# Performance work log

Hardware: AMD Instinct MI355X
Metric: run time of the kernel (lower is better)

The kernel has to match this reference:

```python
import jax, jax.numpy as jnp
import numpy as np

B, F, M, N, H, O = 8, 128, 256, 1024, 64, 128
BN_EPS = 1e-5
COS_EPS = 1e-8


def _bn(x, g, b, m, v):
    # inference-mode BatchNorm over channel axis 1
    shape = [1] * x.ndim
    shape[1] = -1
    return g.reshape(shape) * (x - m.reshape(shape)) * jax.lax.rsqrt(v.reshape(shape) + BN_EPS) + b.reshape(shape)


def setup_inputs() -> dict:
    key = jax.random.key(0)
    ks = jax.random.split(key, 24)
    def n(k, shape, s=1.0):
        return jax.random.normal(k, shape, dtype=jnp.float32) * s
    inp = {}
    inp['template_feature'] = n(ks[0], (B, F, M))
    inp['search_feature'] = n(ks[1], (B, F, N))
    # SharedMLP 1x1 conv weights (bias=False because bn=True)
    inp['W1'] = n(ks[2], (H, F + 1), 0.05)
    inp['W2'] = n(ks[3], (H, H), 0.05)
    inp['W3'] = n(ks[4], (H, H), 0.05)
    # fea_layer: conv1d(H, bn=True) then conv1d(O, activation=None, bias=True)
    inp['Wc1'] = n(ks[5], (H, H), 0.05)
    inp['Wc2'] = n(ks[6], (O, H), 0.05)
    inp['bc2'] = n(ks[7], (O,), 0.05)
    for i, nm in enumerate(['1', '2', '3', 'c1']):
        inp['g' + nm] = 1.0 + n(ks[8 + i], (H,), 0.1)
        inp['b' + nm] = n(ks[12 + i], (H,), 0.1)
        inp['m' + nm] = n(ks[16 + i], (H,), 0.01)
        inp['v' + nm] = jax.random.uniform(ks[20 + i], (H,), minval=0.5, maxval=1.5, dtype=jnp.float32)
    return inp


def reference(template_feature, search_feature, W1, W2, W3, Wc1, Wc2, bc2,
              g1, b1, m1, v1, g2, b2, m2, v2, g3, b3, m3, v3, gc1, bc1, mc1, vc1):
    t, s = template_feature, search_feature
    # pairwise cosine similarity over channel dim (no BxFxMxN expand needed)
    dot = jnp.einsum('bfm,bfn->bmn', t, s)
    nt = jnp.linalg.norm(t, axis=1)  # (B, M)
    ns = jnp.linalg.norm(s, axis=1)  # (B, N)
    cos = dot / jnp.maximum(nt[:, :, None] * ns[:, None, :], COS_EPS)  # (B, M, N)
    # first 1x1 conv on concat(cos, expand(t)) computed fused (no concat materialization)
    h = jnp.einsum('hf,bfm->bhm', W1[:, 1:], t)[..., None] + W1[:, 0][None, :, None, None] * cos[:, None]
    h = jax.nn.relu(_bn(h, g1, b1, m1, v1))  # (B, H, M, N)
    h = jax.nn.relu(_bn(jnp.einsum('gh,bhmn->bgmn', W2, h), g2, b2, m2, v2))
    h = jax.nn.relu(_bn(jnp.einsum('gh,bhmn->bgmn', W3, h), g3, b3, m3, v3))
    p = jnp.max(h, axis=2)  # max-pool over M -> (B, H, N)
    c = jax.nn.relu(_bn(jnp.einsum('gh,bhn->bgn', Wc1, p), gc1, bc1, mc1, vc1))
    return jnp.einsum('oh,bhn->bon', Wc2, c) + bc2[None, :, None]  # (B, O, N)
```

## Files before the change

kernel.cpp:

```cpp
#include <hip/hip_runtime.h>


#define BB 8
#define FF 128
#define MM 256
#define NN 1024
#define HH 64
#define OO 128
#define BN_EPS 1e-5f
#define COS_EPS 1e-8f

#define WS_U     0
#define WS_C2    64
#define WS_C3    128
#define WS_CC1   192
#define WS_W2H   256
#define WS_W3H   2304
#define WS_WC1F  8448
#define WS_A1    12544
#define WS_NT    143616
#define WS_NS    145664
#define WS_COSH  153856
#define WS_P     1202432
#define PS       524288

typedef _Float16 half2v __attribute__((ext_vector_type(2)));
typedef _Float16 half8  __attribute__((ext_vector_type(8)));
typedef __attribute__((ext_vector_type(4))) float f32x4;

__device__ __forceinline__ unsigned int pkh2(float a, float b){
  auto h = __builtin_amdgcn_cvt_pkrtz(a, b);
  return __builtin_bit_cast(unsigned int, h);
}
__device__ __forceinline__ half2v u2h(unsigned int u){
  return __builtin_bit_cast(half2v, u);
}
__device__ __forceinline__ unsigned int h2u(half2v v){
  return __builtin_bit_cast(unsigned int, v);
}
__device__ __forceinline__ unsigned int relu2(unsigned int d){
  half2v v = __builtin_elementwise_max(u2h(d), (half2v){(_Float16)0, (_Float16)0});
  return h2u(v);
}
__device__ __forceinline__ unsigned int bh1(unsigned int up, half2v c, unsigned int ap){
  half2v v = __builtin_elementwise_fma(u2h(up), c, u2h(ap));
  v = __builtin_elementwise_max(v, (half2v){(_Float16)0, (_Float16)0});
  return h2u(v);
}
__device__ __forceinline__ float dot4(float4 a, float4 b, float acc){
  acc = fmaf(a.x, b.x, acc); acc = fmaf(a.y, b.y, acc);
  acc = fmaf(a.z, b.z, acc); acc = fmaf(a.w, b.w, acc);
  return acc;
}

__global__ __launch_bounds__(256) void k_prep(const float* t_, const float* s_,
    const float* W1, const float* W2, const float* W3, const float* Wc1,
    const float* g1, const float* b1, const float* m1, const float* v1,
    const float* g2, const float* b2, const float* m2, const float* v2,
    const float* g3, const float* b3, const float* m3, const float* v3,
    const float* gc1,const float* bc1,const float* mc1,const float* vc1,
    float* ws){
  __shared__ float W1s[64][133];
  int t = threadIdx.x;
  int bx = blockIdx.x;
  if (bx < 256){
    int b = bx >> 5, m0 = (bx & 31)*8;
    for (int idx = t; idx < 8192; idx += 256){
      int h = idx >> 7, f = idx & 127;
      W1s[h][f] = W1[h*129 + 1 + f];
    }
    __syncthreads();
    int h = t & 63, mg = t >> 6;
    const float* tp = t_ + (size_t)b*FF*MM + m0 + mg*2;
    float acc0 = 0.f, acc1 = 0.f;
    for (int f = 0; f < FF; f++){
      float wv = W1s[h][f];
      float2 tv = *(const float2*)&tp[(size_t)f*MM];
      acc0 = fmaf(wv, tv.x, acc0); acc1 = fmaf(wv, tv.y, acc1);
    }
    float a1 = g1[h] / sqrtf(v1[h] + BN_EPS);
    float c1 = b1[h] - a1*m1[h];
    unsigned short* dst = (unsigned short*)(ws + WS_A1) + ((size_t)(b*MM + m0 + mg*2))*64 + h;
    dst[0]  = (unsigned short)(pkh2(fmaf(a1, acc0, c1), 0.f) & 0xFFFFu);
    dst[64] = (unsigned short)(pkh2(fmaf(a1, acc1, c1), 0.f) & 0xFFFFu);
  } else if (bx < 416){
    __shared__ float red[4][64];
    int x = t & 63, fq = t >> 6;
    int idx = (bx - 256)*64 + x;
    const float* ptr; size_t stride;
    if (idx < BB*MM){
      int b = idx >> 8, m = idx & 255;
      ptr = t_ + (size_t)b*FF*MM + m; stride = MM;
    } else {
      int j = idx - BB*MM;
      int b = j >> 10, n = j & 1023;
      ptr = s_ + (size_t)b*FF*NN + n; stride = NN;
    }
    float acc = 0.f;
    for (int f = fq*32; f < fq*32 + 32; f++){
      float v = ptr[(size_t)f*stride]; acc = fmaf(v, v, acc);
    }
    red[fq][x] = acc;
    __syncthreads();
    if (fq == 0)
      ws[WS_NT + idx] = sqrtf(red[0][x] + red[1][x] + red[2][x] + red[3][x]);
  } else {
    if (t < 64){
      float a1 = g1[t] / sqrtf(v1[t] + BN_EPS);
      ws[WS_U + t]   = a1 * W1[t*129];
      float a2 = g2[t] / sqrtf(v2[t] + BN_EPS);
      ws[WS_C2 + t]  = b2[t] - a2*m2[t];
      float a3 = g3[t] / sqrtf(v3[t] + BN_EPS);
      ws[WS_C3 + t]  = b3[t] - a3*m3[t];
      float ac = gc1[t] / sqrtf(vc1[t] + BN_EPS);
      ws[WS_CC1 + t] = bc1[t] - ac*mc1[t];
    }
    unsigned short* w2h = (unsigned short*)(ws + WS_W2H);
    unsigned short* w3h = (unsigned short*)(ws + WS_W3H);
    for (int i = t; i < 4096; i += 256){
      int g = i >> 6;
      float a2 = g2[g] / sqrtf(v2[g] + BN_EPS);
      w2h[i] = __builtin_bit_cast(unsigned short, (_Float16)(a2 * W2[i]));
      float a3 = g3[g] / sqrtf(v3[g] + BN_EPS);
      w3h[i] = __builtin_bit_cast(unsigned short, (_Float16)(a3 * W3[i]));
      float ac = gc1[g] / sqrtf(vc1[g] + BN_EPS);
      ws[WS_WC1F + i] = ac * Wc1[i];
    }
  }
}

__global__ __launch_bounds__(256) void k_cos(const float* t_, const float* s_, float* ws){
  __shared__ __align__(16) unsigned short tS[64][136];
  __shared__ __align__(16) unsigned short sS[64][136];
  __shared__ float ntS[64], nsS[64];
  int t = threadIdx.x;
  int lane = t & 63, w = t >> 6;
  int ln15 = lane & 15, quad = lane >> 4;
  int m0 = blockIdx.x*64, n0 = blockIdx.y*64, b = blockIdx.z;
  {
    int x = t & 63;
    const float* tb = t_ + (size_t)b*FF*MM + m0 + x;
    const float* sb = s_ + (size_t)b*FF*NN + n0 + x;
    #pragma unroll
    for (int k = 0; k < 16; k++){
      int fp = w*16 + k;
      *(unsigned int*)&tS[x][2*fp] = pkh2(tb[(size_t)(2*fp)*MM], tb[(size_t)(2*fp+1)*MM]);
      *(unsigned int*)&sS[x][2*fp] = pkh2(sb[(size_t)(2*fp)*NN], sb[(size_t)(2*fp+1)*NN]);
    }
    if (t < 64) ntS[t] = ws[WS_NT + b*MM + m0 + t];
    else if (t < 128) nsS[t-64] = ws[WS_NS + b*NN + n0 + (t-64)];
  }
  __syncthreads();
  half8 A4[4];
  #pragma unroll
  for (int kc = 0; kc < 4; kc++)
    A4[kc] = *(const half8*)&tS[w*16 + ln15][kc*32 + quad*8];
  float4 nt4 = *(const float4*)&ntS[w*16 + quad*4];
  unsigned short* cosw = (unsigned short*)(ws + WS_COSH);
  #pragma unroll
  for (int ns = 0; ns < 4; ns++){
    f32x4 acc = (f32x4){0.f,0.f,0.f,0.f};
    #pragma unroll
    for (int kc = 0; kc < 4; kc++){
      half8 B4 = *(const half8*)&sS[ns*16 + ln15][kc*32 + quad*8];
      acc = __builtin_amdgcn_mfma_f32_16x16x32_f16(A4[kc], B4, acc, 0, 0, 0);
    }
    float nsv = nsS[ns*16 + ln15];
    int n = n0 + ns*16 + ln15;
    #pragma unroll
    for (int r = 0; r < 4; r++){
      int m = m0 + w*16 + quad*4 + r;
      float denom = fmaxf(nt4[r]*nsv, COS_EPS);
      float c = acc[r] * __builtin_amdgcn_rcpf(denom);
      cosw[(size_t)(b*MM + m)*NN + n] = (unsigned short)(pkh2(c, 0.f) & 0xFFFFu);
    }
  }
}

__global__ __launch_bounds__(256, 3) void k_main(const float* ws, float* Pp){
  __shared__ __align__(16) unsigned short h2W[4][16][72];
  __shared__ __align__(16) float redS[3][16][68];
  int t = threadIdx.x;
  int lane = t & 63, w = t >> 6;
  int ln15 = lane & 15, quad = lane >> 4;
  int b = blockIdx.y;
  int n0 = blockIdx.x * 16;
  int ms = blockIdx.z;

  const unsigned short* w2h = (const unsigned short*)(ws + WS_W2H);
  const unsigned short* w3h = (const unsigned short*)(ws + WS_W3H);
  half8 W2A[4][2], W3A[4][2];
  f32x4 c2v[4], c3v[4];
  #pragma unroll
  for (int rt = 0; rt < 4; rt++){
    int g = rt*16 + ln15;
    #pragma unroll
    for (int kk = 0; kk < 2; kk++){
      W2A[rt][kk] = *(const half8*)&w2h[g*64 + kk*32 + quad*8];
      W3A[rt][kk] = *(const half8*)&w3h[g*64 + kk*32 + quad*8];
    }
    float4 cb2 = *(const float4*)&ws[WS_C2 + rt*16 + quad*4];
    float4 cb3 = *(const float4*)&ws[WS_C3 + rt*16 + quad*4];
    c2v[rt] = (f32x4){cb2.x, cb2.y, cb2.z, cb2.w};
    c3v[rt] = (f32x4){cb3.x, cb3.y, cb3.z, cb3.w};
  }
  unsigned int upk[2][4];
  #pragma unroll
  for (int kk = 0; kk < 2; kk++){
    float4 ua = *(const float4*)&ws[WS_U + kk*32 + quad*8];
    float4 ub = *(const float4*)&ws[WS_U + kk*32 + quad*8 + 4];
    upk[kk][0] = pkh2(ua.x, ua.y); upk[kk][1] = pkh2(ua.z, ua.w);
    upk[kk][2] = pkh2(ub.x, ub.y); upk[kk][3] = pkh2(ub.z, ub.w);
  }
  const unsigned short* A1H = (const unsigned short*)(ws + WS_A1) + (size_t)b*MM*64;
  int n = n0 + ln15;
  const unsigned short* cosP = (const unsigned short*)(ws + WS_COSH)
                               + (size_t)b*MM*NN + n;
  unsigned short* h2w = &h2W[w][0][0];

  f32x4 p[4];
  #pragma unroll
  for (int rt = 0; rt < 4; rt++) p[rt] = (f32x4){0.f,0.f,0.f,0.f};

  int m0i = ms*128 + w;
  unsigned int cu = cosP[(size_t)m0i*NN];
  uint4 a1a = *(const uint4*)&A1H[(size_t)m0i*64 + quad*8];
  uint4 a1b = *(const uint4*)&A1H[(size_t)m0i*64 + 32 + quad*8];

  for (int mc = 0; mc < 32; mc++){
    int mN = ms*128 + (mc < 31 ? (mc + 1) : 31)*4 + w;
    unsigned int cuN = cosP[(size_t)mN*NN];
    uint4 a1aN = *(const uint4*)&A1H[(size_t)mN*64 + quad*8];
    uint4 a1bN = *(const uint4*)&A1H[(size_t)mN*64 + 32 + quad*8];

    unsigned int cd = cu | (cu << 16);
    half2v ch = u2h(cd);
    uint4 q0, q1;
    q0.x = bh1(upk[0][0], ch, a1a.x); q0.y = bh1(upk[0][1], ch, a1a.y);
    q0.z = bh1(upk[0][2], ch, a1a.z); q0.w = bh1(upk[0][3], ch, a1a.w);
    q1.x = bh1(upk[1][0], ch, a1b.x); q1.y = bh1(upk[1][1], ch, a1b.y);
    q1.z = bh1(upk[1][2], ch, a1b.z); q1.w = bh1(upk[1][3], ch, a1b.w);
    half8 b0h = __builtin_bit_cast(half8, q0);
    half8 b1h = __builtin_bit_cast(half8, q1);

    f32x4 acc[4];
    #pragma unroll
    for (int rt = 0; rt < 4; rt++){
      acc[rt] = __builtin_amdgcn_mfma_f32_16x16x32_f16(W2A[rt][0], b0h, c2v[rt], 0, 0, 0);
      acc[rt] = __builtin_amdgcn_mfma_f32_16x16x32_f16(W2A[rt][1], b1h, acc[rt], 0, 0, 0);
    }
    #pragma unroll
    for (int rt = 0; rt < 4; rt++){
      uint2 vv;
      vv.x = relu2(pkh2(acc[rt][0], acc[rt][1]));
      vv.y = relu2(pkh2(acc[rt][2], acc[rt][3]));
      *(uint2*)&h2w[ln15*72 + rt*16 + quad*4] = vv;
    }
    __asm__ volatile("s_waitcnt lgkmcnt(0)" ::: "memory");
    half8 e0 = *(const half8*)&h2w[ln15*72 + quad*8];
    half8 e1 = *(const half8*)&h2w[ln15*72 + 32 + quad*8];
    #pragma unroll
    for (int rt = 0; rt < 4; rt++){
      f32x4 a3 = __builtin_amdgcn_mfma_f32_16x16x32_f16(W3A[rt][0], e0, c3v[rt], 0, 0, 0);
      a3 = __builtin_amdgcn_mfma_f32_16x16x32_f16(W3A[rt][1], e1, a3, 0, 0, 0);
      #pragma unroll
      for (int r = 0; r < 4; r++) p[rt][r] = fmaxf(p[rt][r], a3[r]);
    }
    cu = cuN; a1a = a1aN; a1b = a1bN;
  }

  __syncthreads();
  if (w >= 1){
    #pragma unroll
    for (int rt = 0; rt < 4; rt++){
      f32x4 v = p[rt];
      *(float4*)&redS[w-1][ln15][rt*16 + quad*4] = make_float4(v[0], v[1], v[2], v[3]);
    }
  }
  __syncthreads();
  if (w == 0){
    float* Pb = Pp + (size_t)ms*PS + ((size_t)(b*NN + n) << 6);
    #pragma unroll
    for (int rt = 0; rt < 4; rt++){
      float4 o1 = *(const float4*)&redS[0][ln15][rt*16 + quad*4];
      float4 o2 = *(const float4*)&redS[1][ln15][rt*16 + quad*4];
      float4 o3 = *(const float4*)&redS[2][ln15][rt*16 + quad*4];
      float4 r4;
      r4.x = fmaxf(fmaxf(p[rt][0], o1.x), fmaxf(o2.x, o3.x));
      r4.y = fmaxf(fmaxf(p[rt][1], o1.y), fmaxf(o2.y, o3.y));
      r4.z = fmaxf(fmaxf(p[rt][2], o1.z), fmaxf(o2.z, o3.z));
      r4.w = fmaxf(fmaxf(p[rt][3], o1.w), fmaxf(o2.w, o3.w));
      *(float4*)&Pb[rt*16 + quad*4] = r4;
    }
  }
}

__global__ __launch_bounds__(256) void k_tail(const float* Wc2, const float* bc2,
                                              const float* ws, float* out){
  __shared__ float WT[64][68];
  __shared__ float pT[32][68];
  __shared__ float cS[32][68];
  int t = threadIdx.x;
  int n0 = blockIdx.x * 32;
  int b = blockIdx.y;
  for (int i = t; i < 4096; i += 256) WT[i >> 6][i & 63] = ws[WS_WC1F + i];
  const float* P0 = ws + WS_P + ((size_t)(b*NN + n0) << 6);
  const float* P1 = P0 + PS;
  for (int i = t; i < 2048; i += 256) pT[i >> 6][i & 63] = fmaxf(P0[i], P1[i]);
  __syncthreads();
  {
    int n = t & 31, q = t >> 5;
    for (int k = 0; k < 8; k++){
      int g = q*8 + k;
      float acc = ws[WS_CC1 + g];
      for (int hs = 0; hs < 64; hs += 4){
        float4 wv = *(const float4*)&WT[g][hs];
        float4 pv = *(const float4*)&pT[n][hs];
        acc = dot4(wv, pv, acc);
      }
      cS[n][g] = fmaxf(acc, 0.f);
    }
  }
  __syncthreads();
  {
    int o = t & 127, hf = t >> 7;
    float bco = bc2[o];
    float accO[16];
    #pragma unroll
    for (int i = 0; i < 16; i++) accO[i] = bco;
    for (int hs = 0; hs < 64; hs += 4){
      float4 w4 = *(const float4*)&Wc2[o*64 + hs];
      #pragma unroll
      for (int i = 0; i < 16; i++){
        float4 cv = *(const float4*)&cS[hf*16 + i][hs];
        accO[i] = dot4(w4, cv, accO[i]);
      }
    }
    #pragma unroll
    for (int i = 0; i < 16; i++)
      out[((size_t)(b*OO + o))*NN + n0 + hf*16 + i] = accO[i];
  }
}

extern "C" void kernel_launch(void* const* d_in, const int* in_sizes, int n_in,
                              void* d_out, int out_size, void* d_ws, size_t ws_size,
                              hipStream_t stream){
  (void)in_sizes; (void)n_in; (void)out_size; (void)ws_size;
  const float* t_  = (const float*)d_in[0];
  const float* s_  = (const float*)d_in[1];
  const float* W1  = (const float*)d_in[2];
  const float* W2  = (const float*)d_in[3];
  const float* W3  = (const float*)d_in[4];
  const float* Wc1 = (const float*)d_in[5];
  const float* Wc2 = (const float*)d_in[6];
  const float* bc2 = (const float*)d_in[7];
  const float* g1 = (const float*)d_in[8],  *b1 = (const float*)d_in[9],
             * m1 = (const float*)d_in[10], *v1 = (const float*)d_in[11];
  const float* g2 = (const float*)d_in[12], *b2 = (const float*)d_in[13],
             * m2 = (const float*)d_in[14], *v2 = (const float*)d_in[15];
  const float* g3 = (const float*)d_in[16], *b3 = (const float*)d_in[17],
             * m3 = (const float*)d_in[18], *v3 = (const float*)d_in[19];
  const float* gc1 = (const float*)d_in[20], *bc1 = (const float*)d_in[21],
             * mc1 = (const float*)d_in[22], *vc1 = (const float*)d_in[23];
  float* ws = (float*)d_ws;
  float* out = (float*)d_out;

  k_prep<<<417, 256, 0, stream>>>(t_, s_, W1, W2, W3, Wc1,
      g1,b1,m1,v1, g2,b2,m2,v2, g3,b3,m3,v3, gc1,bc1,mc1,vc1, ws);
  k_cos<<<dim3(4, 16, 8), 256, 0, stream>>>(t_, s_, ws);
  k_main<<<dim3(64, 8, 2), 256, 0, stream>>>(ws, ws + WS_P);
  k_tail<<<dim3(32, 8), 256, 0, stream>>>(Wc2, bc2, ws, out);
}
```

Baseline: 183.2 us.

## Software-pipeline layer2/layer3 MFMAs with double-buffered LDS and defer bias/ReLU past max

Restructures the per-warp M loop so that the layer-3 MFMAs for iteration mc-1 run while the layer-2 MFMAs for iteration mc are issued. Layer-2 results go into a double-buffered LDS staging area with a new padded byte layout, which removes the explicit lgkmcnt wait between the store and reload. The layer-3 bias and ReLU are moved out of the inner loop and applied once after the max reduction, since max commutes with a per-channel add and with ReLU. The running max is now initialised to a large negative value so this stays correct. The change adds a prologue and epilogue and more live registers, which may pressure occupancy under launch_bounds(256,3).

```diff
diff --git a/kernel.cpp b/kernel.cpp
--- a/kernel.cpp
+++ b/kernel.cpp
@@ -178,7 +178,7 @@
 }
 
 __global__ __launch_bounds__(256, 3) void k_main(const float* ws, float* Pp){
-  __shared__ __align__(16) unsigned short h2W[4][16][72];
+  __shared__ __align__(16) unsigned char h2B[4][2][2176];
   __shared__ __align__(16) float redS[3][16][68];
   int t = threadIdx.x;
   int lane = t & 63, w = t >> 6;
@@ -190,7 +190,7 @@
   const unsigned short* w2h = (const unsigned short*)(ws + WS_W2H);
   const unsigned short* w3h = (const unsigned short*)(ws + WS_W3H);
   half8 W2A[4][2], W3A[4][2];
-  f32x4 c2v[4], c3v[4];
+  f32x4 c2v[4];
   #pragma unroll
   for (int rt = 0; rt < 4; rt++){
     int g = rt*16 + ln15;
@@ -200,10 +200,9 @@
       W3A[rt][kk] = *(const half8*)&w3h[g*64 + kk*32 + quad*8];
     }
     float4 cb2 = *(const float4*)&ws[WS_C2 + rt*16 + quad*4];
-    float4 cb3 = *(const float4*)&ws[WS_C3 + rt*16 + quad*4];
     c2v[rt] = (f32x4){cb2.x, cb2.y, cb2.z, cb2.w};
-    c3v[rt] = (f32x4){cb3.x, cb3.y, cb3.z, cb3.w};
-  }
+  }
+  f32x4 zf = (f32x4){0.f, 0.f, 0.f, 0.f};
   unsigned int upk[2][4];
   #pragma unroll
   for (int kk = 0; kk < 2; kk++){
@@ -216,23 +215,25 @@
   int n = n0 + ln15;
   const unsigned short* cosP = (const unsigned short*)(ws + WS_COSH)
                                + (size_t)b*MM*NN + n;
-  unsigned short* h2w = &h2W[w][0][0];
+  unsigned char* myb = &h2B[w][0][0];
+  int wOff = quad*136 + ln15*8;
+  int rOff = quad*272 + ln15*8;
 
   f32x4 p[4];
   #pragma unroll
-  for (int rt = 0; rt < 4; rt++) p[rt] = (f32x4){0.f,0.f,0.f,0.f};
+  for (int rt = 0; rt < 4; rt++)
+    p[rt] = (f32x4){-3.0e38f, -3.0e38f, -3.0e38f, -3.0e38f};
 
   int m0i = ms*128 + w;
   unsigned int cu = cosP[(size_t)m0i*NN];
   uint4 a1a = *(const uint4*)&A1H[(size_t)m0i*64 + quad*8];
   uint4 a1b = *(const uint4*)&A1H[(size_t)m0i*64 + 32 + quad*8];
 
-  for (int mc = 0; mc < 32; mc++){
-    int mN = ms*128 + (mc < 31 ? (mc + 1) : 31)*4 + w;
+  {
+    int mN = ms*128 + 4 + w;
     unsigned int cuN = cosP[(size_t)mN*NN];
     uint4 a1aN = *(const uint4*)&A1H[(size_t)mN*64 + quad*8];
     uint4 a1bN = *(const uint4*)&A1H[(size_t)mN*64 + 32 + quad*8];
-
     unsigned int cd = cu | (cu << 16);
     half2v ch = u2h(cd);
     uint4 q0, q1;
@@ -242,7 +243,6 @@
     q1.z = bh1(upk[1][2], ch, a1b.z); q1.w = bh1(upk[1][3], ch, a1b.w);
     half8 b0h = __builtin_bit_cast(half8, q0);
     half8 b1h = __builtin_bit_cast(half8, q1);
-
     f32x4 acc[4];
     #pragma unroll
     for (int rt = 0; rt < 4; rt++){
@@ -254,19 +254,80 @@
       uint2 vv;
       vv.x = relu2(pkh2(acc[rt][0], acc[rt][1]));
       vv.y = relu2(pkh2(acc[rt][2], acc[rt][3]));
-      *(uint2*)&h2w[ln15*72 + rt*16 + quad*4] = vv;
-    }
-    __asm__ volatile("s_waitcnt lgkmcnt(0)" ::: "memory");
-    half8 e0 = *(const half8*)&h2w[ln15*72 + quad*8];
-    half8 e1 = *(const half8*)&h2w[ln15*72 + 32 + quad*8];
-    #pragma unroll
-    for (int rt = 0; rt < 4; rt++){
-      f32x4 a3 = __builtin_amdgcn_mfma_f32_16x16x32_f16(W3A[rt][0], e0, c3v[rt], 0, 0, 0);
-      a3 = __builtin_amdgcn_mfma_f32_16x16x32_f16(W3A[rt][1], e1, a3, 0, 0, 0);
+      *(uint2*)(myb + rt*544 + wOff) = vv;
+    }
+    cu = cuN; a1a = a1aN; a1b = a1bN;
+  }
+
+  for (int mc = 1; mc < 32; mc++){
+    unsigned char* rb = myb + ((mc - 1) & 1)*2176;
+    uint2 e0l = *(const uint2*)(rb + rOff);
+    uint2 e0h = *(const uint2*)(rb + rOff + 136);
+    uint2 e1l = *(const uint2*)(rb + rOff + 1088);
+    uint2 e1h = *(const uint2*)(rb + rOff + 1224);
+
+    int mN = ms*128 + (mc < 31 ? mc + 1 : 31)*4 + w;
+    unsigned int cuN = cosP[(size_t)mN*NN];
+    uint4 a1aN = *(const uint4*)&A1H[(size_t)mN*64 + quad*8];
+    uint4 a1bN = *(const uint4*)&A1H[(size_t)mN*64 + 32 + quad*8];
+
+    unsigned int cd = cu | (cu << 16);
+    half2v ch = u2h(cd);
+    uint4 q0, q1;
+    q0.x = bh1(upk[0][0], ch, a1a.x); q0.y = bh1(upk[0][1], ch, a1a.y);
+    q0.z = bh1(upk[0][2], ch, a1a.z); q0.w = bh1(upk[0][3], ch, a1a.w);
+    q1.x = bh1(upk[1][0], ch, a1b.x); q1.y = bh1(upk[1][1], ch, a1b.y);
+    q1.z = bh1(upk[1][2], ch, a1b.z); q1.w = bh1(upk[1][3], ch, a1b.w);
+    half8 b0h = __builtin_bit_cast(half8, q0);
+    half8 b1h = __builtin_bit_cast(half8, q1);
+
+    f32x4 acc[4];
+    #pragma unroll
+    for (int rt = 0; rt < 4; rt++){
+      acc[rt] = __builtin_amdgcn_mfma_f32_16x16x32_f16(W2A[rt][0], b0h, c2v[rt], 0, 0, 0);
+      acc[rt] = __builtin_amdgcn_mfma_f32_16x16x32_f16(W2A[rt][1], b1h, acc[rt], 0, 0, 0);
+    }
+
+    uint4 ue0 = make_uint4(e0l.x, e0l.y, e0h.x, e0h.y);
+    uint4 ue1 = make_uint4(e1l.x, e1l.y, e1h.x, e1h.y);
+    half8 pe0 = __builtin_bit_cast(half8, ue0);
+    half8 pe1 = __builtin_bit_cast(half8, ue1);
+    #pragma unroll
+    for (int rt = 0; rt < 4; rt++){
+      f32x4 a3 = __builtin_amdgcn_mfma_f32_16x16x32_f16(W3A[rt][0], pe0, zf, 0, 0, 0);
+      a3 = __builtin_amdgcn_mfma_f32_16x16x32_f16(W3A[rt][1], pe1, a3, 0, 0, 0);
       #pragma unroll
       for (int r = 0; r < 4; r++) p[rt][r] = fmaxf(p[rt][r], a3[r]);
     }
+
+    unsigned char* wb = myb + (mc & 1)*2176;
+    #pragma unroll
+    for (int rt = 0; rt < 4; rt++){
+      uint2 vv;
+      vv.x = relu2(pkh2(acc[rt][0], acc[rt][1]));
+      vv.y = relu2(pkh2(acc[rt][2], acc[rt][3]));
+      *(uint2*)(wb + rt*544 + wOff) = vv;
+    }
     cu = cuN; a1a = a1aN; a1b = a1bN;
+  }
+
+  {
+    unsigned char* rb = myb + 2176;
+    uint2 e0l = *(const uint2*)(rb + rOff);
+    uint2 e0h = *(const uint2*)(rb + rOff + 136);
+    uint2 e1l = *(const uint2*)(rb + rOff + 1088);
+    uint2 e1h = *(const uint2*)(rb + rOff + 1224);
+    uint4 ue0 = make_uint4(e0l.x, e0l.y, e0h.x, e0h.y);
+    uint4 ue1 = make_uint4(e1l.x, e1l.y, e1h.x, e1h.y);
+    half8 pe0 = __builtin_bit_cast(half8, ue0);
+    half8 pe1 = __builtin_bit_cast(half8, ue1);
+    #pragma unroll
+    for (int rt = 0; rt < 4; rt++){
+      f32x4 a3 = __builtin_amdgcn_mfma_f32_16x16x32_f16(W3A[rt][0], pe0, zf, 0, 0, 0);
+      a3 = __builtin_amdgcn_mfma_f32_16x16x32_f16(W3A[rt][1], pe1, a3, 0, 0, 0);
+      #pragma unroll
+      for (int r = 0; r < 4; r++) p[rt][r] = fmaxf(p[rt][r], a3[r]);
+    }
   }
 
   __syncthreads();
@@ -285,11 +346,12 @@
       float4 o1 = *(const float4*)&redS[0][ln15][rt*16 + quad*4];
       float4 o2 = *(const float4*)&redS[1][ln15][rt*16 + quad*4];
       float4 o3 = *(const float4*)&redS[2][ln15][rt*16 + quad*4];
+      float4 c3b = *(const float4*)&ws[WS_C3 + rt*16 + quad*4];
       float4 r4;
-      r4.x = fmaxf(fmaxf(p[rt][0], o1.x), fmaxf(o2.x, o3.x));
-      r4.y = fmaxf(fmaxf(p[rt][1], o1.y), fmaxf(o2.y, o3.y));
-      r4.z = fmaxf(fmaxf(p[rt][2], o1.z), fmaxf(o2.z, o3.z));
-      r4.w = fmaxf(fmaxf(p[rt][3], o1.w), fmaxf(o2.w, o3.w));
+      r4.x = fmaxf(fmaxf(fmaxf(p[rt][0], o1.x), fmaxf(o2.x, o3.x)) + c3b.x, 0.f);
+      r4.y = fmaxf(fmaxf(fmaxf(p[rt][1], o1.y), fmaxf(o2.y, o3.y)) + c3b.y, 0.f);
+      r4.z = fmaxf(fmaxf(fmaxf(p[rt][2], o1.z), fmaxf(o2.z, o3.z)) + c3b.z, 0.f);
+      r4.w = fmaxf(fmaxf(fmaxf(p[rt][3], o1.w), fmaxf(o2.w, o3.w)) + c3b.w, 0.f);
       *(float4*)&Pb[rt*16 + quad*4] = r4;
     }
   }
```

New measurement: 168.7 us. 1.09x faster.
